# Kernel optimization log

Measured on AMD Instinct MI355X. Metric: run time of the kernel, lower is better.

The kernel has to match this reference:

```python
import jax, jax.numpy as jnp
import numpy as np

N, E = 50000, 800000
D_IN, H, D_OUT = 100, 128, 40
N_MID = 2  # num_layers(5) - 3
EPS = 1e-5


def setup_inputs() -> dict:
    key = jax.random.key(0)
    ks = iter(jax.random.split(key, 40))
    rn = lambda shape, s=0.05: jax.random.normal(next(ks), shape, dtype=jnp.float32) * s
    inp = {
        "x": jax.random.normal(next(ks), (N, D_IN), dtype=jnp.float32),
        "edge_index": jax.random.randint(next(ks), (2, E), 0, N, dtype=jnp.int64),
        "percent": 70,
        "ricci_curvature": jax.random.normal(next(ks), (E,), dtype=jnp.float32),
        # GCNConv weights/biases
        "W1": rn((D_IN, H)), "b1": jnp.zeros((H,), jnp.float32),
        "W2": rn((D_IN + H, H)), "b2": jnp.zeros((H,), jnp.float32),
        "Wm": rn((N_MID, 2 * H, H)), "bm": jnp.zeros((N_MID, H), jnp.float32),
        "Wo": rn((2 * H, D_OUT)), "bo": jnp.zeros((D_OUT,), jnp.float32),
    }
    # BatchNorm1d params + running stats (eval mode)
    def bn_params(dim, lead=()):
        return (jnp.ones(lead + (dim,), jnp.float32),            # gamma
                jnp.zeros(lead + (dim,), jnp.float32),           # beta
                rn(lead + (dim,), 0.1),                          # running mean
                1.0 + 0.1 * jax.random.uniform(next(ks), lead + (dim,), dtype=jnp.float32))  # running var
    inp["bn1_g"], inp["bn1_b"], inp["bn1_m"], inp["bn1_v"] = bn_params(D_IN)
    inp["bn2_g"], inp["bn2_b"], inp["bn2_m"], inp["bn2_v"] = bn_params(D_IN + H)
    inp["bnm_g"], inp["bnm_b"], inp["bnm_m"], inp["bnm_v"] = bn_params(2 * H, (N_MID,))
    inp["bno_g"], inp["bno_b"], inp["bno_m"], inp["bno_v"] = bn_params(2 * H)
    return inp


def reference(x, edge_index, percent, ricci_curvature,
              W1, b1, W2, b2, Wm, bm, Wo, bo,
              bn1_g, bn1_b, bn1_m, bn1_v,
              bn2_g, bn2_b, bn2_m, bn2_v,
              bnm_g, bnm_b, bnm_m, bnm_v,
              bno_g, bno_b, bno_m, bno_v):
    # Eval mode: no sampling / dynamic edge weights, dropout = identity,
    # BN uses running stats. GCNConv = PyG: add self-loops, sym-norm D^-1/2 A D^-1/2.
    n = x.shape[0]
    loop = jnp.arange(n)
    src = jnp.concatenate([edge_index[0], loop])  # [E+N]
    dst = jnp.concatenate([edge_index[1], loop])
    deg = jnp.zeros((n,), x.dtype).at[dst].add(1.0)  # >=1 thanks to self-loops
    dis = jax.lax.rsqrt(deg)
    norm = (dis[src] * dis[dst])[:, None]  # [E+N, 1]

    def gcn(h, W, b):
        hw = h @ W  # [N, out]
        agg = jnp.zeros((n, W.shape[1]), h.dtype).at[dst].add(hw[src] * norm)
        return agg + b

    def bn(h, g, bta, m, v):
        return (h - m) * (g * jax.lax.rsqrt(v + EPS)) + bta

    res = []
    x_in = x
    h = jax.nn.relu(gcn(bn(x, bn1_g, bn1_b, bn1_m, bn1_v), W1, b1))
    res.append(h)
    h = jnp.concatenate([h, x_in], axis=1)  # [N, H+D_IN]
    h = jax.nn.relu(gcn(bn(h, bn2_g, bn2_b, bn2_m, bn2_v), W2, b2))
    res.append(h)
    h = jnp.concatenate([h, res[-2]], axis=1)  # [N, 2H]
    for i in range(Wm.shape[0]):
        hi = jax.nn.relu(gcn(bn(h, bnm_g[i], bnm_b[i], bnm_m[i], bnm_v[i]), Wm[i], bm[i]))
        res.append(hi)
        h = jnp.concatenate([hi, res[-2]], axis=1)
    out = gcn(bn(h, bno_g, bno_b, bno_m, bno_v), Wo, bo)
    return (out, *res)
```

## Files before the change

### kernel.cpp

```cpp
#include <hip/hip_runtime.h>
#include <hip/hip_bf16.h>
#include <cstdint>
#include <cstddef>

#define BN_EPS 1e-5f
typedef long long ll;
typedef unsigned short ushortt;
using bf16x8 = __attribute__((ext_vector_type(8))) short;
using f32x4  = __attribute__((ext_vector_type(4))) float;

__device__ __forceinline__ unsigned short f2bf(float f) {
    union { float f; unsigned u; } c; c.f = f;
    unsigned u = c.u;
    u += 0x7fff + ((u >> 16) & 1);
    return (unsigned short)(u >> 16);
}
__device__ __forceinline__ float bf2f(unsigned h) {
    union { unsigned u; float f; } c; c.u = h << 16;
    return c.f;
}
__device__ __forceinline__ void addbf(float* a, uint2 v) {
    a[0] += bf2f(v.x & 0xffffu); a[1] += bf2f(v.x >> 16);
    a[2] += bf2f(v.y & 0xffffu); a[3] += bf2f(v.y >> 16);
}

__global__ __launch_bounds__(1024) void detect_kernel(const int* ei32, int* flag) {
    __shared__ int any;
    if (threadIdx.x == 0) any = 0;
    __syncthreads();
    for (int i = threadIdx.x; i < 2048; i += 1024) {
        if (ei32[2 * i + 1] != 0) any = 1;
    }
    __syncthreads();
    if (threadIdx.x == 0) *flag = (any == 0) ? 1 : 0;
}

__global__ void init_kernel(int* deg, int* cursor, int N) {
    int i = blockIdx.x * 256 + threadIdx.x;
    if (i < N) { deg[i] = 1; cursor[i] = 0; }
}

__global__ void count_kernel(const void* ei, int E, int* deg, const int* flag) {
    int e = blockIdx.x * 256 + threadIdx.x;
    if (e >= E) return;
    int d = (*flag) ? (int)((const ll*)ei)[(size_t)E + e]
                    : ((const int*)ei)[(size_t)E + e];
    atomicAdd(&deg[d], 1);
}

__global__ void dis_kernel(const int* deg, float* dis, int N) {
    int i = blockIdx.x * 256 + threadIdx.x;
    if (i < N) dis[i] = rsqrtf((float)deg[i]);
}

__global__ __launch_bounds__(1024) void scanA_kernel(const int* deg, int* row_ptr,
                                                     int* bsum, int N) {
    __shared__ int wsum[16];
    int i = blockIdx.x * 1024 + threadIdx.x;
    int lane = threadIdx.x & 63, wid = threadIdx.x >> 6;
    int v = (i < N) ? (deg[i] - 1) : 0;
    int s = v;
#pragma unroll
    for (int o = 1; o < 64; o <<= 1) { int t = __shfl_up(s, o); if (lane >= o) s += t; }
    if (lane == 63) wsum[wid] = s;
    __syncthreads();
    if (threadIdx.x < 16) {
        int w = wsum[threadIdx.x];
        int ws_ = w;
#pragma unroll
        for (int o = 1; o < 16; o <<= 1) { int t = __shfl_up(ws_, o); if ((int)threadIdx.x >= o) ws_ += t; }
        wsum[threadIdx.x] = ws_ - w;
    }
    __syncthreads();
    s += wsum[wid];
    if (i < N) row_ptr[i + 1] = s;
    if (threadIdx.x == 1023) bsum[blockIdx.x] = s;
}

__global__ void scanB_kernel(int* bsum, int nb) {
    int lane = threadIdx.x;
    int v = (lane < nb) ? bsum[lane] : 0;
    int s = v;
#pragma unroll
    for (int o = 1; o < 64; o <<= 1) { int t = __shfl_up(s, o); if (lane >= o) s += t; }
    if (lane < nb) bsum[lane] = s - v;
}

__global__ __launch_bounds__(1024) void scanC_kernel(int* row_ptr, const int* bsum, int N) {
    int i = blockIdx.x * 1024 + threadIdx.x;
    if (i < N) row_ptr[i + 1] += bsum[blockIdx.x];
    if (i == 0) row_ptr[0] = 0;
}

__global__ void fill_kernel(const void* ei, int E, const int* row_ptr,
                            int* cursor, int* csr, const int* flag) {
    int e = blockIdx.x * 256 + threadIdx.x;
    if (e >= E) return;
    int s, d;
    if (*flag) { const ll* p = (const ll*)ei; s = (int)p[e]; d = (int)p[(size_t)E + e]; }
    else       { const int* p = (const int*)ei; s = p[e]; d = p[(size_t)E + e]; }
    int pos = atomicAdd(&cursor[d], 1);
    csr[row_ptr[d] + pos] = s;
}

__global__ void fold_b_kernel(const float* __restrict__ W, const float* __restrict__ g,
                              const float* __restrict__ v, unsigned short* __restrict__ Bhi,
                              unsigned short* __restrict__ Blo, int K, int Dout, int ncb) {
    int nkc = (K + 31) >> 5;
    int total = nkc * ncb * 512;
    int idx = blockIdx.x * 256 + threadIdx.x;
    if (idx >= total) return;
    int i = idx & 7;
    int lane = (idx >> 3) & 63;
    int cb = (idx >> 9) % ncb;
    int kc = (idx >> 9) / ncb;
    int k = kc * 32 + (lane >> 4) * 8 + i;
    int col = cb * 16 + (lane & 15);
    float val = 0.f;
    if (k < K && col < Dout) {
        float s = g[k] * rsqrtf(v[k] + BN_EPS);
        val = W[k * Dout + col] * s;
    }
    unsigned short h = f2bf(val);
    Bhi[idx] = h;
    Blo[idx] = f2bf(val - bf2f(h));
}

__global__ __launch_bounds__(256) void fold_c2_kernel(
    const float* __restrict__ W, const float* __restrict__ g,
    const float* __restrict__ bta, const float* __restrict__ m,
    const float* __restrict__ v, float* __restrict__ cvec, int K, int Dout) {
    int wid = threadIdx.x >> 6, lane = threadIdx.x & 63;
    int col = blockIdx.x * 4 + wid;
    float acc = 0.f;
    if (col < Dout) {
        for (int k = lane; k < K; k += 64) {
            float s = g[k] * rsqrtf(v[k] + BN_EPS);
            acc += (bta[k] - m[k] * s) * W[k * Dout + col];
        }
    }
#pragma unroll
    for (int o = 32; o >= 1; o >>= 1) acc += __shfl_xor(acc, o);
    if (lane == 0 && col < 128) cvec[col] = (col < Dout) ? acc : 0.f;
}

template <int NCB, bool BF16OUT>
__global__ __launch_bounds__(256) void gemm_mfma_kernel(
    const float* __restrict__ X1, int K1, int ld1,
    const float* __restrict__ X2, int ld2,
    const unsigned short* __restrict__ Bhi, const unsigned short* __restrict__ Blo,
    const float* __restrict__ cvec, const float* __restrict__ dis,
    void* __restrict__ outp, int ldC, int Dout, int K, int N)
{
    __shared__ float Xs[128 * 32];
    const int tid = threadIdx.x;
    const int w = tid >> 6, lane = tid & 63;
    const int lr = lane & 15, lg = lane >> 4;
    const int brow = blockIdx.x * 128;
    const int nkc = (K + 31) >> 5;

    f32x4 acc[2][NCB];
#pragma unroll
    for (int cb = 0; cb < NCB; ++cb) {
        float cv = cvec[cb * 16 + lr];
        f32x4 iv = {cv, cv, cv, cv};
        acc[0][cb] = iv;
        acc[1][cb] = iv;
    }

    for (int kc = 0; kc < nkc; ++kc) {
        const int k0 = kc * 32;
#pragma unroll
        for (int p = 0; p < 4; ++p) {
            int fidx = (p * 256 + tid) * 4;
            int r = fidx >> 5;
            int c = fidx & 31;
            int grow = brow + r;
            int k = k0 + c;
            float4 val = make_float4(0.f, 0.f, 0.f, 0.f);
            if (grow < N) {
                if (k < K1)      val = *(const float4*)(X1 + (size_t)grow * ld1 + k);
                else if (k < K)  val = *(const float4*)(X2 + (size_t)grow * ld2 + (k - K1));
            }
            *(float4*)((char*)Xs + r * 128 + ((c * 4) ^ ((r & 7) << 4))) = val;
        }
        __syncthreads();

        bf16x8 ahi[2], alo[2];
#pragma unroll
        for (int rb = 0; rb < 2; ++rb) {
            int r = w * 32 + rb * 16 + lr;
            const char* base = (const char*)Xs + r * 128;
            int swz = (r & 7) << 4;
            int cb0 = lg * 32;
            float4 v0 = *(const float4*)(base + (cb0 ^ swz));
            float4 v1 = *(const float4*)(base + ((cb0 + 16) ^ swz));
            float xv[8] = {v0.x, v0.y, v0.z, v0.w, v1.x, v1.y, v1.z, v1.w};
#pragma unroll
            for (int i = 0; i < 8; ++i) {
                unsigned short h = f2bf(xv[i]);
                ahi[rb][i] = (short)h;
                alo[rb][i] = (short)f2bf(xv[i] - bf2f(h));
            }
        }

        const bf16x8* bh = (const bf16x8*)Bhi + (size_t)kc * NCB * 64;
        const bf16x8* bl = (const bf16x8*)Blo + (size_t)kc * NCB * 64;
#pragma unroll
        for (int cb = 0; cb < NCB; ++cb) {
            bf16x8 bhf = bh[cb * 64 + lane];
            bf16x8 blf = bl[cb * 64 + lane];
#pragma unroll
            for (int rb = 0; rb < 2; ++rb) {
                acc[rb][cb] = __builtin_amdgcn_mfma_f32_16x16x32_bf16(ahi[rb], bhf, acc[rb][cb], 0, 0, 0);
                acc[rb][cb] = __builtin_amdgcn_mfma_f32_16x16x32_bf16(ahi[rb], blf, acc[rb][cb], 0, 0, 0);
                acc[rb][cb] = __builtin_amdgcn_mfma_f32_16x16x32_bf16(alo[rb], bhf, acc[rb][cb], 0, 0, 0);
            }
        }
        __syncthreads();
    }

#pragma unroll
    for (int rb = 0; rb < 2; ++rb) {
#pragma unroll
        for (int r = 0; r < 4; ++r) {
            int grow = brow + w * 32 + rb * 16 + lg * 4 + r;
            if (grow >= N) continue;
            float d = dis[grow];
            if (BF16OUT) {
                unsigned short* hb = (unsigned short*)outp;
#pragma unroll
                for (int cb = 0; cb < NCB; ++cb) {
                    int col = cb * 16 + lr;
                    hb[(size_t)grow * 128 + col] = f2bf(d * acc[rb][cb][r]);
                }
            } else {
                float* fo = (float*)outp;
#pragma unroll
                for (int cb = 0; cb < NCB; ++cb) {
                    int col = cb * 16 + lr;
                    if (col < Dout) fo[(size_t)grow * ldC + col] = d * acc[rb][cb][r];
                }
            }
        }
    }
}

template <bool RELU>
__global__ __launch_bounds__(256) void agg128b_kernel(
    const unsigned short* __restrict__ hwb,
    const int* __restrict__ row_ptr, const int* __restrict__ csr,
    const float* __restrict__ dis, const float* __restrict__ bias,
    float* __restrict__ outp, int N)
{
    int wid = threadIdx.x >> 6, lane = threadIdx.x & 63;
    int node = blockIdx.x * 4 + wid;
    if (node >= N) return;
    const int half = lane >> 5, q = lane & 31;
    const uint2* hw2 = (const uint2*)hwb;
    float a[4] = {0.f, 0.f, 0.f, 0.f};
    float b4[4] = {0.f, 0.f, 0.f, 0.f};
    if (half == 0) addbf(a, hw2[(size_t)node * 32 + q]);
    int beg = row_ptr[node], end = row_ptr[node + 1];
    for (int base = beg; base < end; base += 64) {
        int idx = base + lane;
        int j = (idx < end) ? csr[idx] : 0;
        int cnt = end - base; if (cnt > 64) cnt = 64;
        int fullp = cnt >> 1;
        int t = 0;
        for (; t + 4 <= fullp; t += 4) {
            int ja = __shfl(j, 2 * t     + half);
            int jb = __shfl(j, 2 * t + 2 + half);
            int jc = __shfl(j, 2 * t + 4 + half);
            int jd = __shfl(j, 2 * t + 6 + half);
            uint2 va = hw2[(size_t)ja * 32 + q];
            uint2 vb = hw2[(size_t)jb * 32 + q];
            uint2 vc = hw2[(size_t)jc * 32 + q];
            uint2 vd = hw2[(size_t)jd * 32 + q];
            addbf(a, va); addbf(b4, vb); addbf(a, vc); addbf(b4, vd);
        }
        for (; t < fullp; ++t) {
            int ja = __shfl(j, 2 * t + half);
            uint2 va = hw2[(size_t)ja * 32 + q];
            addbf(a, va);
        }
        if (cnt & 1) {
            int ja = __shfl(j, cnt - 1);
            if (half == 0) { uint2 va = hw2[(size_t)ja * 32 + q]; addbf(a, va); }
        }
    }
#pragma unroll
    for (int c = 0; c < 4; ++c) {
        a[c] += b4[c];
        a[c] += __shfl_xor(a[c], 32);
    }
    if (half == 0) {
        float d = dis[node];
        float4 bv = ((const float4*)bias)[q];
        float4 o;
        o.x = fmaf(d, a[0], bv.x);
        o.y = fmaf(d, a[1], bv.y);
        o.z = fmaf(d, a[2], bv.z);
        o.w = fmaf(d, a[3], bv.w);
        if (RELU) {
            o.x = fmaxf(o.x, 0.f); o.y = fmaxf(o.y, 0.f);
            o.z = fmaxf(o.z, 0.f); o.w = fmaxf(o.w, 0.f);
        }
        ((float4*)outp)[(size_t)node * 32 + q] = o;
    }
}

__global__ __launch_bounds__(256) void agg40_kernel(
    const float* __restrict__ hw,
    const int* __restrict__ row_ptr, const int* __restrict__ csr,
    const float* __restrict__ dis, const float* __restrict__ bias,
    float* __restrict__ outp, int N)
{
    int wid = threadIdx.x >> 6, lane = threadIdx.x & 63;
    int node = blockIdx.x * 4 + wid;
    if (node >= N) return;
    bool act = lane < 40;
    float a0 = 0.f, a1 = 0.f, a2 = 0.f, a3 = 0.f;
    if (act) a0 = hw[(size_t)node * 40 + lane];
    int beg = row_ptr[node], end = row_ptr[node + 1];
    for (int base = beg; base < end; base += 64) {
        int idx = base + lane;
        int j = (idx < end) ? csr[idx] : 0;
        int cnt = end - base; if (cnt > 64) cnt = 64;
        int t = 0;
        for (; t + 4 <= cnt; t += 4) {
            int j0 = __shfl(j, t), j1 = __shfl(j, t + 1);
            int j2 = __shfl(j, t + 2), j3 = __shfl(j, t + 3);
            if (act) {
                a0 += hw[(size_t)j0 * 40 + lane];
                a1 += hw[(size_t)j1 * 40 + lane];
                a2 += hw[(size_t)j2 * 40 + lane];
                a3 += hw[(size_t)j3 * 40 + lane];
            }
        }
        for (; t < cnt; ++t) {
            int j0 = __shfl(j, t);
            if (act) a0 += hw[(size_t)j0 * 40 + lane];
        }
    }
    if (act) {
        float s = (a0 + a1) + (a2 + a3);
        outp[(size_t)node * 40 + lane] = fmaf(dis[node], s, bias[lane]);
    }
}

extern "C" void kernel_launch(void* const* d_in, const int* in_sizes, int n_in,
                              void* d_out, int out_size, void* d_ws, size_t ws_size,
                              hipStream_t stream) {
    const int N = in_sizes[0] / 100;
    const int E = in_sizes[1] / 2;

    const float* x   = (const float*)d_in[0];
    const void*  ei  = d_in[1];
    const float* W1  = (const float*)d_in[4];
    const float* b1  = (const float*)d_in[5];
    const float* W2  = (const float*)d_in[6];
    const float* b2  = (const float*)d_in[7];
    const float* Wm  = (const float*)d_in[8];
    const float* bm  = (const float*)d_in[9];
    const float* Wo  = (const float*)d_in[10];
    const float* bo  = (const float*)d_in[11];
    const float* bn1g = (const float*)d_in[12];
    const float* bn1b = (const float*)d_in[13];
    const float* bn1m = (const float*)d_in[14];
    const float* bn1v = (const float*)d_in[15];
    const float* bn2g = (const float*)d_in[16];
    const float* bn2b = (const float*)d_in[17];
    const float* bn2m = (const float*)d_in[18];
    const float* bn2v = (const float*)d_in[19];
    const float* bnmg = (const float*)d_in[20];
    const float* bnmb = (const float*)d_in[21];
    const float* bnmm = (const float*)d_in[22];
    const float* bnmv = (const float*)d_in[23];
    const float* bnog = (const float*)d_in[24];
    const float* bnob = (const float*)d_in[25];
    const float* bnom = (const float*)d_in[26];
    const float* bnov = (const float*)d_in[27];

    char* wsb = (char*)d_ws;
    size_t off = 0;
    auto alloc = [&](size_t elems) -> void* { void* p = wsb + off; off += elems * 4; return p; };
    int*   deg     = (int*)alloc(N);
    int*   cursor  = (int*)alloc(N);
    int*   row_ptr = (int*)alloc((size_t)N + 1);
    int*   bsum    = (int*)alloc(64);
    int*   flag    = (int*)alloc(1);
    off = (off + 15) & ~(size_t)15;
    float* dis  = (float*)alloc(N);
    int*   csr  = (int*)alloc(E);
    off = (off + 15) & ~(size_t)15;
    float* hw   = (float*)alloc((size_t)N * 128);
    unsigned short* hwb = (unsigned short*)hw;
    unsigned short* BhiA = (unsigned short*)alloc(63488);
    unsigned short* BloA = (unsigned short*)alloc(63488);
    float* cvecA = (float*)alloc(128 * 5);
    (void)ws_size; (void)n_in; (void)out_size;

    float* outF = (float*)d_out;
    float* h1 = outF + (size_t)N * 40;
    float* h2 = h1 + (size_t)N * 128;
    float* h3 = h2 + (size_t)N * 128;
    float* h4 = h3 + (size_t)N * 128;

    dim3 b256(256);

    const int Boff[5]  = {0, 16384, 49152, 81920, 114688};
    struct FoldP { const float *W, *g, *b, *m, *v; int K, Dout, ncb; };
    FoldP fp[5] = {
        {W1, bn1g, bn1b, bn1m, bn1v, 100, 128, 8},
        {W2, bn2g, bn2b, bn2m, bn2v, 228, 128, 8},
        {Wm, bnmg, bnmb, bnmm, bnmv, 256, 128, 8},
        {Wm + 256 * 128, bnmg + 256, bnmb + 256, bnmm + 256, bnmv + 256, 256, 128, 8},
        {Wo, bnog, bnob, bnom, bnov, 256, 40, 3},
    };
    for (int l = 0; l < 5; ++l) {
        int nkc = (fp[l].K + 31) / 32;
        int ftotal = nkc * fp[l].ncb * 512;
        fold_b_kernel<<<dim3((ftotal + 255) / 256), b256, 0, stream>>>(
            fp[l].W, fp[l].g, fp[l].v, BhiA + Boff[l], BloA + Boff[l], fp[l].K, fp[l].Dout, fp[l].ncb);
        fold_c2_kernel<<<dim3(32), b256, 0, stream>>>(
            fp[l].W, fp[l].g, fp[l].b, fp[l].m, fp[l].v, cvecA + 128 * l, fp[l].K, fp[l].Dout);
    }

    detect_kernel<<<1, 1024, 0, stream>>>((const int*)ei, flag);
    init_kernel<<<dim3((N + 255) / 256), b256, 0, stream>>>(deg, cursor, N);
    count_kernel<<<dim3((E + 255) / 256), b256, 0, stream>>>(ei, E, deg, flag);
    dis_kernel<<<dim3((N + 255) / 256), b256, 0, stream>>>(deg, dis, N);
    int nb = (N + 1023) / 1024;
    scanA_kernel<<<dim3(nb), dim3(1024), 0, stream>>>(deg, row_ptr, bsum, N);
    scanB_kernel<<<1, 64, 0, stream>>>(bsum, nb);
    scanC_kernel<<<dim3(nb), dim3(1024), 0, stream>>>(row_ptr, bsum, N);
    fill_kernel<<<dim3((E + 255) / 256), b256, 0, stream>>>(ei, E, row_ptr, cursor, csr, flag);

    int gemm_grid = (N + 127) / 128;
    int agg_grid  = (N + 3) / 4;

    auto layer = [&](int l, const float* X1, int K1, int ld1, const float* X2, int ld2,
                     const float* lb, int Dout, float* dst, bool relu) {
        int K = fp[l].K;
        const unsigned short* Bhi = BhiA + Boff[l];
        const unsigned short* Blo = BloA + Boff[l];
        const float* cv = cvecA + 128 * l;
        if (Dout == 128) {
            gemm_mfma_kernel<8, true><<<dim3(gemm_grid), b256, 0, stream>>>(
                X1, K1, ld1, X2, ld2, Bhi, Blo, cv, dis, hwb, 128, Dout, K, N);
            if (relu)
                agg128b_kernel<true><<<dim3(agg_grid), b256, 0, stream>>>(hwb, row_ptr, csr, dis, lb, dst, N);
            else
                agg128b_kernel<false><<<dim3(agg_grid), b256, 0, stream>>>(hwb, row_ptr, csr, dis, lb, dst, N);
        } else {
            gemm_mfma_kernel<3, false><<<dim3(gemm_grid), b256, 0, stream>>>(
                X1, K1, ld1, X2, ld2, Bhi, Blo, cv, dis, hw, 40, Dout, K, N);
            agg40_kernel<<<dim3(agg_grid), b256, 0, stream>>>(hw, row_ptr, csr, dis, lb, dst, N);
        }
    };

    layer(0, x, 100, 100, nullptr, 0, b1, 128, h1, true);
    layer(1, h1, 128, 128, x, 100, b2, 128, h2, true);
    layer(2, h2, 128, 128, h1, 128, bm, 128, h3, true);
    layer(3, h3, 128, 128, h2, 128, bm + 128, 128, h4, true);
    layer(4, h4, 128, 128, h3, 128, bo, 40, outF, false);
}
```

Baseline: 442.8 us.

## Feed GEMMs bf16 copies of hidden activations and drop low-part MFMA

The aggregation kernel now also writes a bf16 copy of each layer's output. Later GEMMs read these copies, which halves their input bandwidth, and skip the A-low split MFMA because bf16 inputs have no low part. The final layer's hw is stored as bf16 and aggregated by a new half-wave-split agg40 kernel. The per-layer fold kernels are merged into two batched launches and the dis kernel is folded into the scan. Reading activations at bf16 precision in later layers lowers accuracy relative to the fp32 hi/lo split.

```diff
diff --git a/kernel.cpp b/kernel.cpp
--- a/kernel.cpp
+++ b/kernel.cpp
@@ -5,7 +5,6 @@
 
 #define BN_EPS 1e-5f
 typedef long long ll;
-typedef unsigned short ushortt;
 using bf16x8 = __attribute__((ext_vector_type(8))) short;
 using f32x4  = __attribute__((ext_vector_type(4))) float;
 
@@ -22,6 +21,10 @@
 __device__ __forceinline__ void addbf(float* a, uint2 v) {
     a[0] += bf2f(v.x & 0xffffu); a[1] += bf2f(v.x >> 16);
     a[2] += bf2f(v.y & 0xffffu); a[3] += bf2f(v.y >> 16);
+}
+__device__ __forceinline__ float4 bf4_to_f4(uint2 v) {
+    return make_float4(bf2f(v.x & 0xffffu), bf2f(v.x >> 16),
+                       bf2f(v.y & 0xffffu), bf2f(v.y >> 16));
 }
 
 __global__ __launch_bounds__(1024) void detect_kernel(const int* ei32, int* flag) {
@@ -48,17 +51,14 @@
     atomicAdd(&deg[d], 1);
 }
 
-__global__ void dis_kernel(const int* deg, float* dis, int N) {
-    int i = blockIdx.x * 256 + threadIdx.x;
-    if (i < N) dis[i] = rsqrtf((float)deg[i]);
-}
-
 __global__ __launch_bounds__(1024) void scanA_kernel(const int* deg, int* row_ptr,
-                                                     int* bsum, int N) {
+                                                     int* bsum, float* dis, int N) {
     __shared__ int wsum[16];
     int i = blockIdx.x * 1024 + threadIdx.x;
     int lane = threadIdx.x & 63, wid = threadIdx.x >> 6;
-    int v = (i < N) ? (deg[i] - 1) : 0;
+    int dv = (i < N) ? deg[i] : 1;
+    if (i < N) dis[i] = rsqrtf((float)dv);
+    int v = (i < N) ? (dv - 1) : 0;
     int s = v;
 #pragma unroll
     for (int o = 1; o < 64; o <<= 1) { int t = __shfl_up(s, o); if (lane >= o) s += t; }
@@ -103,54 +103,59 @@
     csr[row_ptr[d] + pos] = s;
 }
 
-__global__ void fold_b_kernel(const float* __restrict__ W, const float* __restrict__ g,
-                              const float* __restrict__ v, unsigned short* __restrict__ Bhi,
-                              unsigned short* __restrict__ Blo, int K, int Dout, int ncb) {
-    int nkc = (K + 31) >> 5;
-    int total = nkc * ncb * 512;
+struct LayerP {
+    const float *W, *g, *b, *m, *v;
+    int K, Dout, ncb, boff;
+};
+struct LayerPs { LayerP l[5]; };
+
+__global__ __launch_bounds__(256) void fold_b_all(LayerPs P,
+                                                  unsigned short* __restrict__ Bhi,
+                                                  unsigned short* __restrict__ Blo) {
+    const LayerP& L = P.l[blockIdx.y];
+    int nkc = (L.K + 31) >> 5;
+    int total = nkc * L.ncb * 512;
     int idx = blockIdx.x * 256 + threadIdx.x;
     if (idx >= total) return;
     int i = idx & 7;
     int lane = (idx >> 3) & 63;
-    int cb = (idx >> 9) % ncb;
-    int kc = (idx >> 9) / ncb;
+    int cb = (idx >> 9) % L.ncb;
+    int kc = (idx >> 9) / L.ncb;
     int k = kc * 32 + (lane >> 4) * 8 + i;
     int col = cb * 16 + (lane & 15);
     float val = 0.f;
-    if (k < K && col < Dout) {
-        float s = g[k] * rsqrtf(v[k] + BN_EPS);
-        val = W[k * Dout + col] * s;
+    if (k < L.K && col < L.Dout) {
+        float s = L.g[k] * rsqrtf(L.v[k] + BN_EPS);
+        val = L.W[k * L.Dout + col] * s;
     }
     unsigned short h = f2bf(val);
-    Bhi[idx] = h;
-    Blo[idx] = f2bf(val - bf2f(h));
-}
-
-__global__ __launch_bounds__(256) void fold_c2_kernel(
-    const float* __restrict__ W, const float* __restrict__ g,
-    const float* __restrict__ bta, const float* __restrict__ m,
-    const float* __restrict__ v, float* __restrict__ cvec, int K, int Dout) {
+    Bhi[L.boff + idx] = h;
+    Blo[L.boff + idx] = f2bf(val - bf2f(h));
+}
+
+__global__ __launch_bounds__(256) void fold_c_all(LayerPs P, float* __restrict__ cvecA) {
+    const LayerP& L = P.l[blockIdx.y];
     int wid = threadIdx.x >> 6, lane = threadIdx.x & 63;
     int col = blockIdx.x * 4 + wid;
     float acc = 0.f;
-    if (col < Dout) {
-        for (int k = lane; k < K; k += 64) {
-            float s = g[k] * rsqrtf(v[k] + BN_EPS);
-            acc += (bta[k] - m[k] * s) * W[k * Dout + col];
+    if (col < L.Dout) {
+        for (int k = lane; k < L.K; k += 64) {
+            float s = L.g[k] * rsqrtf(L.v[k] + BN_EPS);
+            acc += (L.b[k] - L.m[k] * s) * L.W[k * L.Dout + col];
         }
     }
 #pragma unroll
     for (int o = 32; o >= 1; o >>= 1) acc += __shfl_xor(acc, o);
-    if (lane == 0 && col < 128) cvec[col] = (col < Dout) ? acc : 0.f;
-}
-
-template <int NCB, bool BF16OUT>
-__global__ __launch_bounds__(256) void gemm_mfma_kernel(
-    const float* __restrict__ X1, int K1, int ld1,
-    const float* __restrict__ X2, int ld2,
+    if (lane == 0 && col < 128) cvecA[128 * blockIdx.y + col] = (col < L.Dout) ? acc : 0.f;
+}
+
+template <int NCB, bool B1, bool B2>
+__global__ __launch_bounds__(256) void gemm_mix_kernel(
+    const void* __restrict__ X1, int K1, int ld1,
+    const void* __restrict__ X2, int ld2,
     const unsigned short* __restrict__ Bhi, const unsigned short* __restrict__ Blo,
     const float* __restrict__ cvec, const float* __restrict__ dis,
-    void* __restrict__ outp, int ldC, int Dout, int K, int N)
+    unsigned short* __restrict__ outp, int ldH, int Dout, int K, int kc_lo, int N)
 {
     __shared__ float Xs[128 * 32];
     const int tid = threadIdx.x;
@@ -170,6 +175,7 @@
 
     for (int kc = 0; kc < nkc; ++kc) {
         const int k0 = kc * 32;
+        const bool need_lo = (kc >= kc_lo);
 #pragma unroll
         for (int p = 0; p < 4; ++p) {
             int fidx = (p * 256 + tid) * 4;
@@ -179,8 +185,14 @@
             int k = k0 + c;
             float4 val = make_float4(0.f, 0.f, 0.f, 0.f);
             if (grow < N) {
-                if (k < K1)      val = *(const float4*)(X1 + (size_t)grow * ld1 + k);
-                else if (k < K)  val = *(const float4*)(X2 + (size_t)grow * ld2 + (k - K1));
+                if (k < K1) {
+                    if (B1) val = bf4_to_f4(*(const uint2*)((const unsigned short*)X1 + (size_t)grow * ld1 + k));
+                    else    val = *(const float4*)((const float*)X1 + (size_t)grow * ld1 + k);
+                } else if (k < K) {
+                    int kk = k - K1;
+                    if (B2) val = bf4_to_f4(*(const uint2*)((const unsigned short*)X2 + (size_t)grow * ld2 + kk));
+                    else    val = *(const float4*)((const float*)X2 + (size_t)grow * ld2 + kk);
+                }
             }
             *(float4*)((char*)Xs + r * 128 + ((c * 4) ^ ((r & 7) << 4))) = val;
         }
@@ -200,7 +212,7 @@
             for (int i = 0; i < 8; ++i) {
                 unsigned short h = f2bf(xv[i]);
                 ahi[rb][i] = (short)h;
-                alo[rb][i] = (short)f2bf(xv[i] - bf2f(h));
+                alo[rb][i] = need_lo ? (short)f2bf(xv[i] - bf2f(h)) : (short)0;
             }
         }
 
@@ -214,7 +226,8 @@
             for (int rb = 0; rb < 2; ++rb) {
                 acc[rb][cb] = __builtin_amdgcn_mfma_f32_16x16x32_bf16(ahi[rb], bhf, acc[rb][cb], 0, 0, 0);
                 acc[rb][cb] = __builtin_amdgcn_mfma_f32_16x16x32_bf16(ahi[rb], blf, acc[rb][cb], 0, 0, 0);
-                acc[rb][cb] = __builtin_amdgcn_mfma_f32_16x16x32_bf16(alo[rb], bhf, acc[rb][cb], 0, 0, 0);
+                if (need_lo)
+                    acc[rb][cb] = __builtin_amdgcn_mfma_f32_16x16x32_bf16(alo[rb], bhf, acc[rb][cb], 0, 0, 0);
             }
         }
         __syncthreads();
@@ -227,20 +240,90 @@
             int grow = brow + w * 32 + rb * 16 + lg * 4 + r;
             if (grow >= N) continue;
             float d = dis[grow];
-            if (BF16OUT) {
-                unsigned short* hb = (unsigned short*)outp;
-#pragma unroll
-                for (int cb = 0; cb < NCB; ++cb) {
-                    int col = cb * 16 + lr;
-                    hb[(size_t)grow * 128 + col] = f2bf(d * acc[rb][cb][r]);
-                }
-            } else {
-                float* fo = (float*)outp;
-#pragma unroll
-                for (int cb = 0; cb < NCB; ++cb) {
-                    int col = cb * 16 + lr;
-                    if (col < Dout) fo[(size_t)grow * ldC + col] = d * acc[rb][cb][r];
-                }
+#pragma unroll
+            for (int cb = 0; cb < NCB; ++cb) {
+                int col = cb * 16 + lr;
+                if (col < Dout) outp[(size_t)grow * ldH + col] = f2bf(d * acc[rb][cb][r]);
+            }
+        }
+    }
+}
+
+template <int NCB>
+__global__ __launch_bounds__(256) void gemm_bf_kernel(
+    const unsigned short* __restrict__ X1, int K1, int ld1,
+    const unsigned short* __restrict__ X2, int ld2,
+    const unsigned short* __restrict__ Bhi, const unsigned short* __restrict__ Blo,
+    const float* __restrict__ cvec, const float* __restrict__ dis,
+    unsigned short* __restrict__ outp, int ldH, int Dout, int K, int N)
+{
+    __shared__ unsigned short Xs[128 * 32];
+    const int tid = threadIdx.x;
+    const int w = tid >> 6, lane = tid & 63;
+    const int lr = lane & 15, lg = lane >> 4;
+    const int brow = blockIdx.x * 128;
+    const int nkc = (K + 31) >> 5;
+
+    f32x4 acc[2][NCB];
+#pragma unroll
+    for (int cb = 0; cb < NCB; ++cb) {
+        float cv = cvec[cb * 16 + lr];
+        f32x4 iv = {cv, cv, cv, cv};
+        acc[0][cb] = iv;
+        acc[1][cb] = iv;
+    }
+
+    for (int kc = 0; kc < nkc; ++kc) {
+        const int k0 = kc * 32;
+#pragma unroll
+        for (int p = 0; p < 2; ++p) {
+            int idx8 = p * 256 + tid;
+            int r = idx8 >> 2;
+            int cq = idx8 & 3;
+            int grow = brow + r;
+            int k = k0 + cq * 8;
+            uint4 raw = make_uint4(0, 0, 0, 0);
+            if (grow < N) {
+                if (k < K1)      raw = *(const uint4*)(X1 + (size_t)grow * ld1 + k);
+                else if (k < K)  raw = *(const uint4*)(X2 + (size_t)grow * ld2 + (k - K1));
+            }
+            *(uint4*)((char*)Xs + r * 64 + ((cq * 16) ^ ((r & 3) << 4))) = raw;
+        }
+        __syncthreads();
+
+        bf16x8 ahi[2];
+#pragma unroll
+        for (int rb = 0; rb < 2; ++rb) {
+            int r = w * 32 + rb * 16 + lr;
+            ahi[rb] = *(const bf16x8*)((const char*)Xs + r * 64 + ((lg * 16) ^ ((r & 3) << 4)));
+        }
+
+        const bf16x8* bh = (const bf16x8*)Bhi + (size_t)kc * NCB * 64;
+        const bf16x8* bl = (const bf16x8*)Blo + (size_t)kc * NCB * 64;
+#pragma unroll
+        for (int cb = 0; cb < NCB; ++cb) {
+            bf16x8 bhf = bh[cb * 64 + lane];
+            bf16x8 blf = bl[cb * 64 + lane];
+#pragma unroll
+            for (int rb = 0; rb < 2; ++rb) {
+                acc[rb][cb] = __builtin_amdgcn_mfma_f32_16x16x32_bf16(ahi[rb], bhf, acc[rb][cb], 0, 0, 0);
+                acc[rb][cb] = __builtin_amdgcn_mfma_f32_16x16x32_bf16(ahi[rb], blf, acc[rb][cb], 0, 0, 0);
+            }
+        }
+        __syncthreads();
+    }
+
+#pragma unroll
+    for (int rb = 0; rb < 2; ++rb) {
+#pragma unroll
+        for (int r = 0; r < 4; ++r) {
+            int grow = brow + w * 32 + rb * 16 + lg * 4 + r;
+            if (grow >= N) continue;
+            float d = dis[grow];
+#pragma unroll
+            for (int cb = 0; cb < NCB; ++cb) {
+                int col = cb * 16 + lr;
+                if (col < Dout) outp[(size_t)grow * ldH + col] = f2bf(d * acc[rb][cb][r]);
             }
         }
     }
@@ -251,7 +334,7 @@
     const unsigned short* __restrict__ hwb,
     const int* __restrict__ row_ptr, const int* __restrict__ csr,
     const float* __restrict__ dis, const float* __restrict__ bias,
-    float* __restrict__ outp, int N)
+    float* __restrict__ outp, unsigned short* __restrict__ hbout, int N)
 {
     int wid = threadIdx.x >> 6, lane = threadIdx.x & 63;
     int node = blockIdx.x * 4 + wid;
@@ -307,11 +390,15 @@
             o.z = fmaxf(o.z, 0.f); o.w = fmaxf(o.w, 0.f);
         }
         ((float4*)outp)[(size_t)node * 32 + q] = o;
-    }
-}
-
-__global__ __launch_bounds__(256) void agg40_kernel(
-    const float* __restrict__ hw,
+        uint2 pk;
+        pk.x = (unsigned)f2bf(o.x) | ((unsigned)f2bf(o.y) << 16);
+        pk.y = (unsigned)f2bf(o.z) | ((unsigned)f2bf(o.w) << 16);
+        ((uint2*)hbout)[(size_t)node * 32 + q] = pk;
+    }
+}
+
+__global__ __launch_bounds__(256) void agg40b_kernel(
+    const unsigned short* __restrict__ hwb,
     const int* __restrict__ row_ptr, const int* __restrict__ csr,
     const float* __restrict__ dis, const float* __restrict__ bias,
     float* __restrict__ outp, int N)
@@ -319,33 +406,61 @@
     int wid = threadIdx.x >> 6, lane = threadIdx.x & 63;
     int node = blockIdx.x * 4 + wid;
     if (node >= N) return;
-    bool act = lane < 40;
-    float a0 = 0.f, a1 = 0.f, a2 = 0.f, a3 = 0.f;
-    if (act) a0 = hw[(size_t)node * 40 + lane];
+    const int half = lane >> 5, q = lane & 31;
+    const bool act = q < 20;
+    const unsigned* hw20 = (const unsigned*)hwb;
+    float a0 = 0.f, a1 = 0.f, b0 = 0.f, b1 = 0.f;
+    if (half == 0 && act) {
+        unsigned v = hw20[(size_t)node * 20 + q];
+        a0 += bf2f(v & 0xffffu); a1 += bf2f(v >> 16);
+    }
     int beg = row_ptr[node], end = row_ptr[node + 1];
     for (int base = beg; base < end; base += 64) {
         int idx = base + lane;
         int j = (idx < end) ? csr[idx] : 0;
         int cnt = end - base; if (cnt > 64) cnt = 64;
+        int fullp = cnt >> 1;
         int t = 0;
-        for (; t + 4 <= cnt; t += 4) {
-            int j0 = __shfl(j, t), j1 = __shfl(j, t + 1);
-            int j2 = __shfl(j, t + 2), j3 = __shfl(j, t + 3);
+        for (; t + 4 <= fullp; t += 4) {
+            int ja = __shfl(j, 2 * t     + half);
+            int jb = __shfl(j, 2 * t + 2 + half);
+            int jc = __shfl(j, 2 * t + 4 + half);
+            int jd = __shfl(j, 2 * t + 6 + half);
             if (act) {
-                a0 += hw[(size_t)j0 * 40 + lane];
-                a1 += hw[(size_t)j1 * 40 + lane];
-                a2 += hw[(size_t)j2 * 40 + lane];
-                a3 += hw[(size_t)j3 * 40 + lane];
-            }
-        }
-        for (; t < cnt; ++t) {
-            int j0 = __shfl(j, t);
-            if (act) a0 += hw[(size_t)j0 * 40 + lane];
-        }
-    }
-    if (act) {
-        float s = (a0 + a1) + (a2 + a3);
-        outp[(size_t)node * 40 + lane] = fmaf(dis[node], s, bias[lane]);
+                unsigned va = hw20[(size_t)ja * 20 + q];
+                unsigned vb = hw20[(size_t)jb * 20 + q];
+                unsigned vc = hw20[(size_t)jc * 20 + q];
+                unsigned vd = hw20[(size_t)jd * 20 + q];
+                a0 += bf2f(va & 0xffffu); a1 += bf2f(va >> 16);
+                b0 += bf2f(vb & 0xffffu); b1 += bf2f(vb >> 16);
+                a0 += bf2f(vc & 0xffffu); a1 += bf2f(vc >> 16);
+                b0 += bf2f(vd & 0xffffu); b1 += bf2f(vd >> 16);
+            }
+        }
+        for (; t < fullp; ++t) {
+            int ja = __shfl(j, 2 * t + half);
+            if (act) {
+                unsigned va = hw20[(size_t)ja * 20 + q];
+                a0 += bf2f(va & 0xffffu); a1 += bf2f(va >> 16);
+            }
+        }
+        if (cnt & 1) {
+            int ja = __shfl(j, cnt - 1);
+            if (half == 0 && act) {
+                unsigned va = hw20[(size_t)ja * 20 + q];
+                a0 += bf2f(va & 0xffffu); a1 += bf2f(va >> 16);
+            }
+        }
+    }
+    a0 += b0; a1 += b1;
+    a0 += __shfl_xor(a0, 32);
+    a1 += __shfl_xor(a1, 32);
+    if (half == 0 && act) {
+        float d = dis[node];
+        float2 o;
+        o.x = fmaf(d, a0, bias[2 * q]);
+        o.y = fmaf(d, a1, bias[2 * q + 1]);
+        *(float2*)(outp + (size_t)node * 40 + 2 * q) = o;
     }
 }
 
@@ -394,8 +509,10 @@
     float* dis  = (float*)alloc(N);
     int*   csr  = (int*)alloc(E);
     off = (off + 15) & ~(size_t)15;
-    float* hw   = (float*)alloc((size_t)N * 128);
-    unsigned short* hwb = (unsigned short*)hw;
+    unsigned short* hwb = (unsigned short*)alloc((size_t)N * 64);
+    unsigned short* hbA = (unsigned short*)alloc((size_t)N * 64);
+    unsigned short* hbB = (unsigned short*)alloc((size_t)N * 64);
+    unsigned short* hbC = (unsigned short*)alloc((size_t)N * 64);
     unsigned short* BhiA = (unsigned short*)alloc(63488);
     unsigned short* BloA = (unsigned short*)alloc(63488);
     float* cvecA = (float*)alloc(128 * 5);
@@ -409,30 +526,20 @@
 
     dim3 b256(256);
 
-    const int Boff[5]  = {0, 16384, 49152, 81920, 114688};
-    struct FoldP { const float *W, *g, *b, *m, *v; int K, Dout, ncb; };
-    FoldP fp[5] = {
-        {W1, bn1g, bn1b, bn1m, bn1v, 100, 128, 8},
-        {W2, bn2g, bn2b, bn2m, bn2v, 228, 128, 8},
-        {Wm, bnmg, bnmb, bnmm, bnmv, 256, 128, 8},
-        {Wm + 256 * 128, bnmg + 256, bnmb + 256, bnmm + 256, bnmv + 256, 256, 128, 8},
-        {Wo, bnog, bnob, bnom, bnov, 256, 40, 3},
-    };
-    for (int l = 0; l < 5; ++l) {
-        int nkc = (fp[l].K + 31) / 32;
-        int ftotal = nkc * fp[l].ncb * 512;
-        fold_b_kernel<<<dim3((ftotal + 255) / 256), b256, 0, stream>>>(
-            fp[l].W, fp[l].g, fp[l].v, BhiA + Boff[l], BloA + Boff[l], fp[l].K, fp[l].Dout, fp[l].ncb);
-        fold_c2_kernel<<<dim3(32), b256, 0, stream>>>(
-            fp[l].W, fp[l].g, fp[l].b, fp[l].m, fp[l].v, cvecA + 128 * l, fp[l].K, fp[l].Dout);
-    }
+    LayerPs P;
+    P.l[0] = {W1, bn1g, bn1b, bn1m, bn1v, 100, 128, 8, 0};
+    P.l[1] = {W2, bn2g, bn2b, bn2m, bn2v, 228, 128, 8, 16384};
+    P.l[2] = {Wm, bnmg, bnmb, bnmm, bnmv, 256, 128, 8, 49152};
+    P.l[3] = {Wm + 256 * 128, bnmg + 256, bnmb + 256, bnmm + 256, bnmv + 256, 256, 128, 8, 81920};
+    P.l[4] = {Wo, bnog, bnob, bnom, bnov, 256, 40, 3, 114688};
+    fold_b_all<<<dim3(128, 5), b256, 0, stream>>>(P, BhiA, BloA);
+    fold_c_all<<<dim3(32, 5), b256, 0, stream>>>(P, cvecA);
 
     detect_kernel<<<1, 1024, 0, stream>>>((const int*)ei, flag);
     init_kernel<<<dim3((N + 255) / 256), b256, 0, stream>>>(deg, cursor, N);
     count_kernel<<<dim3((E + 255) / 256), b256, 0, stream>>>(ei, E, deg, flag);
-    dis_kernel<<<dim3((N + 255) / 256), b256, 0, stream>>>(deg, dis, N);
     int nb = (N + 1023) / 1024;
-    scanA_kernel<<<dim3(nb), dim3(1024), 0, stream>>>(deg, row_ptr, bsum, N);
+    scanA_kernel<<<dim3(nb), dim3(1024), 0, stream>>>(deg, row_ptr, bsum, dis, N);
     scanB_kernel<<<1, 64, 0, stream>>>(bsum, nb);
     scanC_kernel<<<dim3(nb), dim3(1024), 0, stream>>>(row_ptr, bsum, N);
     fill_kernel<<<dim3((E + 255) / 256), b256, 0, stream>>>(ei, E, row_ptr, cursor, csr, flag);
@@ -440,29 +547,33 @@
     int gemm_grid = (N + 127) / 128;
     int agg_grid  = (N + 3) / 4;
 
-    auto layer = [&](int l, const float* X1, int K1, int ld1, const float* X2, int ld2,
-                     const float* lb, int Dout, float* dst, bool relu) {
-        int K = fp[l].K;
-        const unsigned short* Bhi = BhiA + Boff[l];
-        const unsigned short* Blo = BloA + Boff[l];
-        const float* cv = cvecA + 128 * l;
-        if (Dout == 128) {
-            gemm_mfma_kernel<8, true><<<dim3(gemm_grid), b256, 0, stream>>>(
-                X1, K1, ld1, X2, ld2, Bhi, Blo, cv, dis, hwb, 128, Dout, K, N);
-            if (relu)
-                agg128b_kernel<true><<<dim3(agg_grid), b256, 0, stream>>>(hwb, row_ptr, csr, dis, lb, dst, N);
-            else
-                agg128b_kernel<false><<<dim3(agg_grid), b256, 0, stream>>>(hwb, row_ptr, csr, dis, lb, dst, N);
-        } else {
-            gemm_mfma_kernel<3, false><<<dim3(gemm_grid), b256, 0, stream>>>(
-                X1, K1, ld1, X2, ld2, Bhi, Blo, cv, dis, hw, 40, Dout, K, N);
-            agg40_kernel<<<dim3(agg_grid), b256, 0, stream>>>(hw, row_ptr, csr, dis, lb, dst, N);
-        }
+    auto agg128 = [&](const float* lb, float* dst, unsigned short* hbout) {
+        agg128b_kernel<true><<<dim3(agg_grid), b256, 0, stream>>>(
+            hwb, row_ptr, csr, dis, lb, dst, hbout, N);
     };
 
-    layer(0, x, 100, 100, nullptr, 0, b1, 128, h1, true);
-    layer(1, h1, 128, 128, x, 100, b2, 128, h2, true);
-    layer(2, h2, 128, 128, h1, 128, bm, 128, h3, true);
-    layer(3, h3, 128, 128, h2, 128, bm + 128, 128, h4, true);
-    layer(4, h4, 128, 128, h3, 128, bo, 40, outF, false);
-}
+    gemm_mix_kernel<8, false, false><<<dim3(gemm_grid), b256, 0, stream>>>(
+        x, 100, 100, nullptr, 0, BhiA + P.l[0].boff, BloA + P.l[0].boff,
+        cvecA, dis, hwb, 128, 128, 100, 0, N);
+    agg128(b1, h1, hbA);
+
+    gemm_mix_kernel<8, true, false><<<dim3(gemm_grid), b256, 0, stream>>>(
+        hbA, 128, 128, x, 100, BhiA + P.l[1].boff, BloA + P.l[1].boff,
+        cvecA + 128, dis, hwb, 128, 128, 228, 4, N);
+    agg128(b2, h2, hbB);
+
+    gemm_bf_kernel<8><<<dim3(gemm_grid), b256, 0, stream>>>(
+        hbB, 128, 128, hbA, 128, BhiA + P.l[2].boff, BloA + P.l[2].boff,
+        cvecA + 256, dis, hwb, 128, 128, 256, N);
+    agg128(bm, h3, hbC);
+
+    gemm_bf_kernel<8><<<dim3(gemm_grid), b256, 0, stream>>>(
+        hbC, 128, 128, hbB, 128, BhiA + P.l[3].boff, BloA + P.l[3].boff,
+        cvecA + 384, dis, hwb, 128, 128, 256, N);
+    agg128(bm + 128, h4, hbA);
+
+    gemm_bf_kernel<3><<<dim3(gemm_grid), b256, 0, stream>>>(
+        hbA, 128, 128, hbC, 128, BhiA + P.l[4].boff, BloA + P.l[4].boff,
+        cvecA + 512, dis, hwb, 40, 40, 256, N);
+    agg40b_kernel<<<dim3(agg_grid), b256, 0, stream>>>(hwb, row_ptr, csr, dis, bo, outF, N);
+}
```

After: 454.7 us. 2.7% more time.
